# Kernel tuning notes

Measured on AMD Instinct MI355X. Metric: run time of the kernel, lower is better.

Reference implementation:

```python
import jax, jax.numpy as jnp
import numpy as np

B, N = 32, 512
NB_TAU, NB_G, NB_W = 8, 8, 6
FLOOR = 0.001
SLOPE_RANGE = (0.5, 4.0)
BIAS_RANGE = (-2.0, 2.0)


def _basis(x, nb, kind):
    # MonotoneBasis: fixed grid of slopes/biases, monotone activation per basis.
    slopes = jnp.asarray(np.linspace(SLOPE_RANGE[0], SLOPE_RANGE[1], nb), x.dtype)
    biases = jnp.asarray(np.linspace(BIAS_RANGE[0], BIAS_RANGE[1], nb), x.dtype)
    z = x[..., None] * slopes + biases  # [..., nb]
    return jax.nn.softplus(z) if kind == 'softplus' else jax.nn.sigmoid(z)


def _normalize_scores(scores, mask, eps=1e-6):
    scores = jnp.where(mask, scores, 0.0)
    denom = jnp.clip(mask.sum(axis=1, keepdims=True), 1)
    mean = scores.sum(axis=1, keepdims=True) / denom
    scores = scores - mean
    var = (scores ** 2 * mask).sum(axis=1, keepdims=True) / denom
    return scores / jnp.sqrt(var + eps)


def setup_inputs() -> dict:
    key = jax.random.key(0)
    k1, k2, k3, k4, k5 = jax.random.split(key, 5)
    return {
        'predictions': jax.random.normal(k1, (B, N), dtype=jnp.float32),
        # targets in [0,1): all valid (no -1 padding), ties have measure zero
        'targets': jax.random.uniform(k2, (B, N), dtype=jnp.float32),
        'theta_tau': jax.random.normal(k3, (NB_TAU,), dtype=jnp.float32) * 0.1,
        'theta_g': jax.random.normal(k4, (NB_G,), dtype=jnp.float32) * 0.1,
        'theta_w': jax.random.normal(k5, (NB_W,), dtype=jnp.float32) * 0.1,
    }


def reference(predictions, targets, theta_tau, theta_g, theta_w):
    mask = ~jnp.isclose(targets, -1.0)
    s = _normalize_scores(predictions, mask)
    r = targets
    n = predictions.shape[1]
    iu, ju = np.triu_indices(n, k=1)  # static pair enumeration, P = n*(n-1)/2

    dr = r[:, iu] - r[:, ju]                      # [B, P]
    t = jnp.sign(dr)
    keep = (t != 0) & mask[:, iu] & mask[:, ju]   # drop ties / padded pairs
    ds = s[:, iu] - s[:, ju]
    abs_dr = jnp.abs(dr)

    # learned nonnegative combination coefficients (monotone outputs)
    c_tau = jax.nn.softplus(theta_tau)
    c_g = jax.nn.softplus(theta_g)
    c_w = jax.nn.softplus(theta_w)

    tau = _basis(abs_dr, NB_TAU, 'softplus') @ c_tau   # learned margin
    m = tau - t * ds
    g = _basis(m, NB_G, 'softplus') @ c_g              # learned penalty
    w = FLOOR + _basis(abs_dr, NB_W, 'sigmoid') @ c_w  # learned gap weight
    pair_loss = g * w

    kf = keep.astype(pair_loss.dtype)
    denom = jnp.clip(kf.sum(axis=1), 1.0)
    row_loss = (pair_loss * kf).sum(axis=1) / denom    # per-row mean over kept pairs
    valid_row = (kf.sum(axis=1) > 0).astype(pair_loss.dtype)
    return (row_loss * valid_row).sum() / jnp.clip(valid_row.sum(), 1.0)
```

## Files before the change

### kernel.cpp

```cpp
#include <hip/hip_runtime.h>
#include <math.h>

#define BB 32
#define NN 512
#define PP 130816
#define KBLK 64
#define TAILSUB (KBLK - 2)

#define OFF_RS2 0
#define OFF_CF  32768
#define OFF_SUM 32816
#define OFF_CNT 32848

__device__ __forceinline__ float splus(float z) {
    return fmaxf(z, 0.0f) + __logf(1.0f + __expf(-fabsf(z)));
}

__device__ __constant__ float ST8[8] = {0.5f, 1.0f, 1.5f, 2.0f, 2.5f, 3.0f, 3.5f, 4.0f};
__device__ __constant__ float BT8[8] = {
    (float)(-2.0), (float)(-2.0 + 4.0/7.0), (float)(-2.0 + 8.0/7.0),
    (float)(-2.0 + 12.0/7.0), (float)(-2.0 + 16.0/7.0),
    (float)(-2.0 + 20.0/7.0), (float)(-2.0 + 24.0/7.0), 2.0f };
__device__ __constant__ float SW6[6] = {0.5f, (float)(0.5 + 3.5/5.0), (float)(0.5 + 7.0/5.0),
    (float)(0.5 + 10.5/5.0), (float)(0.5 + 14.0/5.0), 4.0f};
__device__ __constant__ float BW6[6] = {-2.0f, (float)(-2.0 + 4.0/5.0), (float)(-2.0 + 8.0/5.0),
    (float)(-2.0 + 12.0/5.0), (float)(-2.0 + 16.0/5.0), 2.0f};

__device__ __constant__ float TC[10][10] = {
    {1,0,0,0,0,0,0,0,0,0},
    {0,1,0,0,0,0,0,0,0,0},
    {-1,0,2,0,0,0,0,0,0,0},
    {0,-3,0,4,0,0,0,0,0,0},
    {1,0,-8,0,8,0,0,0,0,0},
    {0,5,0,-20,0,16,0,0,0,0},
    {-1,0,18,0,-48,0,32,0,0,0},
    {0,-7,0,56,0,-112,0,64,0,0},
    {1,0,-32,0,160,0,-256,0,128,0},
    {0,9,0,-120,0,432,0,-576,0,256},
};

__global__ __launch_bounds__(256)
void prep_kernel(const float* __restrict__ pred, const float* __restrict__ targ,
                 const float* __restrict__ th_tau, const float* __restrict__ th_g,
                 const float* __restrict__ th_w, float* __restrict__ ws)
{
    const int bid = blockIdx.x, tid = threadIdx.x;
    if (bid < BB) {
        const int base = bid * NN;
        float x0 = pred[base + tid], x1 = pred[base + tid + 256];
        float t0 = targ[base + tid], t1 = targ[base + tid + 256];
        bool v0 = fabsf(t0 + 1.0f) > 1.00001e-5f;
        bool v1 = fabsf(t1 + 1.0f) > 1.00001e-5f;
        float m0 = v0 ? 1.0f : 0.0f, m1 = v1 ? 1.0f : 0.0f;
        float xs0 = x0 * m0, xs1 = x1 * m1;
        float lsum = xs0 + xs1;
        float lsq  = xs0 * xs0 + xs1 * xs1;
        float lcnt = m0 + m1;
        #pragma unroll
        for (int off = 32; off; off >>= 1) {
            lsum += __shfl_down(lsum, off);
            lsq  += __shfl_down(lsq,  off);
            lcnt += __shfl_down(lcnt, off);
        }
        __shared__ float red[3][4];
        const int lane = tid & 63, wv = tid >> 6;
        if (lane == 0) { red[0][wv] = lsum; red[1][wv] = lsq; red[2][wv] = lcnt; }
        __syncthreads();
        __shared__ float mean_s, rsig_s;
        if (tid == 0) {
            float S = 0.0f, Q = 0.0f, C = 0.0f;
            for (int i = 0; i < 4; i++) { S += red[0][i]; Q += red[1][i]; C += red[2][i]; }
            float denom = fmaxf(C, 1.0f);
            float mean = S / denom;
            float var = Q / denom - mean * mean;
            mean_s = mean;
            rsig_s = 1.0f / sqrtf(var + 1e-6f);
            ws[OFF_SUM + bid] = 0.0f;
            ws[OFF_CNT + bid] = 0.0f;
        }
        __syncthreads();
        const float qnan = __uint_as_float(0x7fc00000u);
        float2* RS2 = (float2*)(ws + OFF_RS2);
        RS2[base + tid]       = make_float2(v0 ? t0 : qnan, (xs0 - mean_s) * rsig_s);
        RS2[base + tid + 256] = make_float2(v1 ? t1 : qnan, (xs1 - mean_s) * rsig_s);
    } else {
        const int wv = tid >> 6, lane = tid & 63;
        __shared__ float fbuf[4][64];
        __shared__ float cbuf[4][10];
        const float mids[4]  = {0.5f, 0.5f, -8.0f, 8.0f};
        const float halfs[4] = {0.5f, 0.5f,  8.0f, 8.0f};
        const int   ncs[4]   = {6, 6, 10, 10};
        const int   bases[4] = {0, 6, 12, 22};
        float u = __cosf((float)M_PI * ((float)lane + 0.5f) * (1.0f / 64.0f));
        float xv = fmaf(halfs[wv], u, mids[wv]);
        float f;
        if (wv == 0) {
            f = 0.0f;
            #pragma unroll
            for (int k = 0; k < 8; k++)
                f = fmaf(splus(fmaf(xv, ST8[k], BT8[k])), splus(th_tau[k]), f);
        } else if (wv == 1) {
            f = 0.001f;
            #pragma unroll
            for (int k = 0; k < 6; k++) {
                float z = fmaf(xv, SW6[k], BW6[k]);
                f = fmaf(1.0f / (1.0f + __expf(-z)), splus(th_w[k]), f);
            }
        } else {
            f = 0.0f;
            #pragma unroll
            for (int k = 0; k < 8; k++)
                f = fmaf(splus(fmaf(xv, ST8[k], BT8[k])), splus(th_g[k]), f);
        }
        fbuf[wv][lane] = f;
        __syncthreads();
        const int nc = ncs[wv];
        if (lane < nc) {
            float c = 0.0f;
            for (int i = 0; i < 64; i++)
                c += fbuf[wv][i] * __cosf((float)M_PI * (float)lane * ((float)i + 0.5f) * (1.0f / 64.0f));
            c *= (lane == 0) ? (1.0f / 64.0f) : (2.0f / 64.0f);
            cbuf[wv][lane] = c;
        }
        __syncthreads();
        if (lane < nc) {
            float mono = 0.0f;
            for (int j = 0; j < nc; j++) mono += cbuf[wv][j] * TC[j][lane];
            ws[OFF_CF + bases[wv] + lane] = mono;
        }
        if (wv == 2 && lane == 0) {
            float gB = 0.0f;
            #pragma unroll
            for (int k = 0; k < 8; k++) gB += splus(th_g[k]) * ST8[k];
            ws[OFF_CF + 32] = gB;
        }
    }
}

__global__ __launch_bounds__(256)
void pair_kernel(float* __restrict__ ws)
{
    const int b   = blockIdx.x & (BB - 1);
    const int sub = blockIdx.x >> 5;
    const int tid = threadIdx.x;
    __shared__ float2 sRS[NN];

    const float2* RS2 = (const float2*)(ws + OFF_RS2);
    sRS[tid]       = RS2[b * NN + tid];
    sRS[tid + 256] = RS2[b * NN + tid + 256];

    float ct[6], cw[6], cn[10], cp[10];
    #pragma unroll
    for (int k = 0; k < 6; k++)  ct[k] = ws[OFF_CF + k];
    #pragma unroll
    for (int k = 0; k < 6; k++)  cw[k] = ws[OFF_CF + 6 + k];
    #pragma unroll
    for (int k = 0; k < 10; k++) cn[k] = ws[OFF_CF + 12 + k];
    #pragma unroll
    for (int k = 0; k < 10; k++) cp[k] = ws[OFF_CF + 22 + k];
    const float gB = ws[OFF_CF + 32];
    __syncthreads();

    float lsum = 0.0f, lcnt = 0.0f;

    auto do_pair = [&](float2 a, float2 q) {
        float dr  = a.x - q.x;
        float ds  = a.y - q.y;
        float tds = __uint_as_float(__float_as_uint(ds) ^
                                    (__float_as_uint(dr) & 0x80000000u));
        float t1  = fmaf(fabsf(dr), 2.0f, -1.0f);
        float tau = fmaf(ct[5], t1, ct[4]);
        tau = fmaf(tau, t1, ct[3]); tau = fmaf(tau, t1, ct[2]);
        tau = fmaf(tau, t1, ct[1]); tau = fmaf(tau, t1, ct[0]);
        float w = fmaf(cw[5], t1, cw[4]);
        w = fmaf(w, t1, cw[3]); w = fmaf(w, t1, cw[2]);
        w = fmaf(w, t1, cw[1]); w = fmaf(w, t1, cw[0]);
        float m  = tau - tds;
        float um = fminf(fmaxf(m, -16.0f), 16.0f);
        bool neg = m < 0.0f;
        float tg = fmaf(um, 0.125f, neg ? 1.0f : -1.0f);
        float g = neg ? cn[9] : cp[9];
        #pragma unroll
        for (int k = 8; k >= 0; k--)
            g = fmaf(g, tg, neg ? cn[k] : cp[k]);
        g = fmaf(fmaxf(m - 16.0f, 0.0f), gB, g);
        float p = g * w;
        bool keep = __builtin_islessgreater(dr, 0.0f);
        lsum = keep ? (lsum + p) : lsum;
        lcnt = keep ? (lcnt + 1.0f) : lcnt;
    };

    const int d0 = (sub >> 1) + 1;
    const int x  = ((sub & 1) << 8) + tid;
    const float2 rsi = sRS[x];
    int j = (x + d0) & (NN - 1);
    const int nIter = (sub >= TAILSUB) ? (PP / (KBLK * 256) - 1) : (PP / (KBLK * 256));
    for (int it = 0; it < nIter; it++) {
        float2 rsj = sRS[j];
        do_pair(rsi, rsj);
        j = (j + 32) & (NN - 1);
    }
    if (sub == TAILSUB) {
        do_pair(sRS[tid], sRS[tid + 256]);
    }

    #pragma unroll
    for (int off = 32; off; off >>= 1) {
        lsum += __shfl_down(lsum, off);
        lcnt += __shfl_down(lcnt, off);
    }
    __shared__ float red[2][4];
    const int lane = tid & 63, wv = tid >> 6;
    if (lane == 0) { red[0][wv] = lsum; red[1][wv] = lcnt; }
    __syncthreads();
    if (tid == 0) {
        float S = red[0][0] + red[0][1] + red[0][2] + red[0][3];
        float C = red[1][0] + red[1][1] + red[1][2] + red[1][3];
        atomicAdd(ws + OFF_SUM + b, S);
        atomicAdd(ws + OFF_CNT + b, C);
    }
}

__global__ void final_kernel(const float* __restrict__ ws, float* __restrict__ out)
{
    const int tid = threadIdx.x;
    float val = 0.0f, vld = 0.0f;
    if (tid < BB) {
        float c = ws[OFF_CNT + tid], s = ws[OFF_SUM + tid];
        float rl = s / fmaxf(c, 1.0f);
        float v  = (c > 0.0f) ? 1.0f : 0.0f;
        val = rl * v;
        vld = v;
    }
    #pragma unroll
    for (int off = 32; off; off >>= 1) {
        val += __shfl_down(val, off);
        vld += __shfl_down(vld, off);
    }
    if (tid == 0) out[0] = val / fmaxf(vld, 1.0f);
}

extern "C" void kernel_launch(void* const* d_in, const int* in_sizes, int n_in,
                              void* d_out, int out_size, void* d_ws, size_t ws_size,
                              hipStream_t stream) {
    const float* pred   = (const float*)d_in[0];
    const float* targ   = (const float*)d_in[1];
    const float* th_tau = (const float*)d_in[2];
    const float* th_g   = (const float*)d_in[3];
    const float* th_w   = (const float*)d_in[4];
    float* ws  = (float*)d_ws;
    float* out = (float*)d_out;

    prep_kernel<<<BB + 1, 256, 0, stream>>>(pred, targ, th_tau, th_g, th_w, ws);
    pair_kernel<<<BB * KBLK, 256, 0, stream>>>(ws);
    final_kernel<<<1, 64, 0, stream>>>(ws, out);
}
```

Measured before the change: 86.62 us.

## Split g polynomial into even/odd parts and reshape pair enumeration

Replaces the sign-dependent Chebyshev selection for g with even and odd polynomial fits in |m|, so two independent Horner chains are combined by a sign flip. This removes the per-coefficient selects, which diverge inside a wavefront. Pair enumeration now uses a 768-entry wrapped shared array and 32 blocks per row, each with 16 fully unrolled contiguous offsets, in place of the modular stride loop and separate tail block. Fewer blocks and more work per thread cut launch and reduction overhead, but the doubled Horner FMA count adds ALU work.

Result: faster. 76.74 us (-11.4%).

```diff
diff --git a/kernel.cpp b/kernel.cpp
--- a/kernel.cpp
+++ b/kernel.cpp
@@ -3,14 +3,11 @@
 
 #define BB 32
 #define NN 512
-#define PP 130816
-#define KBLK 64
-#define TAILSUB (KBLK - 2)
 
 #define OFF_RS2 0
 #define OFF_CF  32768
-#define OFF_SUM 32816
-#define OFF_CNT 32848
+#define OFF_SUM 32808
+#define OFF_CNT 32840
 
 __device__ __forceinline__ float splus(float z) {
     return fmaxf(z, 0.0f) + __logf(1.0f + __expf(-fabsf(z)));
@@ -87,19 +84,16 @@
         const int wv = tid >> 6, lane = tid & 63;
         __shared__ float fbuf[4][64];
         __shared__ float cbuf[4][10];
-        const float mids[4]  = {0.5f, 0.5f, -8.0f, 8.0f};
-        const float halfs[4] = {0.5f, 0.5f,  8.0f, 8.0f};
-        const int   ncs[4]   = {6, 6, 10, 10};
-        const int   bases[4] = {0, 6, 12, 22};
         float u = __cosf((float)M_PI * ((float)lane + 0.5f) * (1.0f / 64.0f));
-        float xv = fmaf(halfs[wv], u, mids[wv]);
         float f;
         if (wv == 0) {
+            float xv = fmaf(0.5f, u, 0.5f);
             f = 0.0f;
             #pragma unroll
             for (int k = 0; k < 8; k++)
                 f = fmaf(splus(fmaf(xv, ST8[k], BT8[k])), splus(th_tau[k]), f);
         } else if (wv == 1) {
+            float xv = fmaf(0.5f, u, 0.5f);
             f = 0.001f;
             #pragma unroll
             for (int k = 0; k < 6; k++) {
@@ -107,14 +101,20 @@
                 f = fmaf(1.0f / (1.0f + __expf(-z)), splus(th_w[k]), f);
             }
         } else {
-            f = 0.0f;
-            #pragma unroll
-            for (int k = 0; k < 8; k++)
-                f = fmaf(splus(fmaf(xv, ST8[k], BT8[k])), splus(th_g[k]), f);
+            float xv = fmaf(8.0f, u, 8.0f);
+            float gp = 0.0f, gn = 0.0f;
+            #pragma unroll
+            for (int k = 0; k < 8; k++) {
+                float c = splus(th_g[k]);
+                gp = fmaf(splus(fmaf( xv, ST8[k], BT8[k])), c, gp);
+                gn = fmaf(splus(fmaf(-xv, ST8[k], BT8[k])), c, gn);
+            }
+            f = (wv == 2) ? 0.5f * (gp + gn) : 0.5f * (gp - gn);
         }
         fbuf[wv][lane] = f;
         __syncthreads();
-        const int nc = ncs[wv];
+        const int nc   = (wv < 2) ? 6 : 10;
+        const int base = (wv == 0) ? 0 : (wv == 1) ? 6 : (wv == 2) ? 12 : 22;
         if (lane < nc) {
             float c = 0.0f;
             for (int i = 0; i < 64; i++)
@@ -126,7 +126,7 @@
         if (lane < nc) {
             float mono = 0.0f;
             for (int j = 0; j < nc; j++) mono += cbuf[wv][j] * TC[j][lane];
-            ws[OFF_CF + bases[wv] + lane] = mono;
+            ws[OFF_CF + base + lane] = mono;
         }
         if (wv == 2 && lane == 0) {
             float gB = 0.0f;
@@ -138,36 +138,36 @@
 }
 
 __global__ __launch_bounds__(256)
-void pair_kernel(float* __restrict__ ws)
+void pair_kernel(const float2* __restrict__ RS2, const float* __restrict__ CF,
+                 float* __restrict__ sums)
 {
     const int b   = blockIdx.x & (BB - 1);
     const int sub = blockIdx.x >> 5;
     const int tid = threadIdx.x;
-    __shared__ float2 sRS[NN];
-
-    const float2* RS2 = (const float2*)(ws + OFF_RS2);
+    __shared__ float2 sRS[768];
     sRS[tid]       = RS2[b * NN + tid];
     sRS[tid + 256] = RS2[b * NN + tid + 256];
-
-    float ct[6], cw[6], cn[10], cp[10];
-    #pragma unroll
-    for (int k = 0; k < 6; k++)  ct[k] = ws[OFF_CF + k];
-    #pragma unroll
-    for (int k = 0; k < 6; k++)  cw[k] = ws[OFF_CF + 6 + k];
-    #pragma unroll
-    for (int k = 0; k < 10; k++) cn[k] = ws[OFF_CF + 12 + k];
-    #pragma unroll
-    for (int k = 0; k < 10; k++) cp[k] = ws[OFF_CF + 22 + k];
-    const float gB = ws[OFF_CF + 32];
+    sRS[tid + 512] = RS2[b * NN + tid];
+
+    float ct[6], cw[6], ce[10], co[10];
+    #pragma unroll
+    for (int k = 0; k < 6; k++)  ct[k] = CF[k];
+    #pragma unroll
+    for (int k = 0; k < 6; k++)  cw[k] = CF[6 + k];
+    #pragma unroll
+    for (int k = 0; k < 10; k++) ce[k] = CF[12 + k];
+    #pragma unroll
+    for (int k = 0; k < 10; k++) co[k] = CF[22 + k];
+    const float gB = CF[32];
     __syncthreads();
 
     float lsum = 0.0f, lcnt = 0.0f;
 
-    auto do_pair = [&](float2 a, float2 q) {
+    auto do_pair = [&](float2 a, float2 q, bool allow) {
         float dr  = a.x - q.x;
         float ds  = a.y - q.y;
-        float tds = __uint_as_float(__float_as_uint(ds) ^
-                                    (__float_as_uint(dr) & 0x80000000u));
+        unsigned sgn = __float_as_uint(dr) & 0x80000000u;
+        float tds = __uint_as_float(__float_as_uint(ds) ^ sgn);
         float t1  = fmaf(fabsf(dr), 2.0f, -1.0f);
         float tau = fmaf(ct[5], t1, ct[4]);
         tau = fmaf(tau, t1, ct[3]); tau = fmaf(tau, t1, ct[2]);
@@ -176,33 +176,36 @@
         w = fmaf(w, t1, cw[3]); w = fmaf(w, t1, cw[2]);
         w = fmaf(w, t1, cw[1]); w = fmaf(w, t1, cw[0]);
         float m  = tau - tds;
-        float um = fminf(fmaxf(m, -16.0f), 16.0f);
-        bool neg = m < 0.0f;
-        float tg = fmaf(um, 0.125f, neg ? 1.0f : -1.0f);
-        float g = neg ? cn[9] : cp[9];
+        float au = fminf(fabsf(m), 16.0f);
+        float tg = fmaf(au, 0.125f, -1.0f);
+        float E = ce[9], O = co[9];
         #pragma unroll
-        for (int k = 8; k >= 0; k--)
-            g = fmaf(g, tg, neg ? cn[k] : cp[k]);
+        for (int k = 8; k >= 0; k--) {
+            E = fmaf(E, tg, ce[k]);
+            O = fmaf(O, tg, co[k]);
+        }
+        unsigned msgn = __float_as_uint(m) & 0x80000000u;
+        float g = E + __uint_as_float(__float_as_uint(O) ^ msgn);
         g = fmaf(fmaxf(m - 16.0f, 0.0f), gB, g);
         float p = g * w;
-        bool keep = __builtin_islessgreater(dr, 0.0f);
+        bool keep = __builtin_islessgreater(dr, 0.0f) && allow;
         lsum = keep ? (lsum + p) : lsum;
         lcnt = keep ? (lcnt + 1.0f) : lcnt;
     };
 
-    const int d0 = (sub >> 1) + 1;
-    const int x  = ((sub & 1) << 8) + tid;
-    const float2 rsi = sRS[x];
-    int j = (x + d0) & (NN - 1);
-    const int nIter = (sub >= TAILSUB) ? (PP / (KBLK * 256) - 1) : (PP / (KBLK * 256));
-    for (int it = 0; it < nIter; it++) {
-        float2 rsj = sRS[j];
-        do_pair(rsi, rsj);
-        j = (j + 32) & (NN - 1);
-    }
-    if (sub == TAILSUB) {
-        do_pair(sRS[tid], sRS[tid + 256]);
-    }
+    const int d0 = sub * 8 + 1;
+    const float2 a0 = sRS[tid];
+    const float2 a1 = sRS[tid + 256];
+    const float2* pj0 = &sRS[tid + d0];
+    const float2* pj1 = &sRS[tid + 256 + d0];
+    const bool lastsub = (sub == 31);
+    #pragma unroll
+    for (int k = 0; k < 8; k++)
+        do_pair(a0, pj0[k], true);
+    #pragma unroll
+    for (int k = 0; k < 7; k++)
+        do_pair(a1, pj1[k], true);
+    do_pair(a1, pj1[7], !lastsub);
 
     #pragma unroll
     for (int off = 32; off; off >>= 1) {
@@ -216,17 +219,17 @@
     if (tid == 0) {
         float S = red[0][0] + red[0][1] + red[0][2] + red[0][3];
         float C = red[1][0] + red[1][1] + red[1][2] + red[1][3];
-        atomicAdd(ws + OFF_SUM + b, S);
-        atomicAdd(ws + OFF_CNT + b, C);
-    }
-}
-
-__global__ void final_kernel(const float* __restrict__ ws, float* __restrict__ out)
+        atomicAdd(sums + b, S);
+        atomicAdd(sums + BB + b, C);
+    }
+}
+
+__global__ void final_kernel(const float* __restrict__ sums, float* __restrict__ out)
 {
     const int tid = threadIdx.x;
     float val = 0.0f, vld = 0.0f;
     if (tid < BB) {
-        float c = ws[OFF_CNT + tid], s = ws[OFF_SUM + tid];
+        float s = sums[tid], c = sums[BB + tid];
         float rl = s / fmaxf(c, 1.0f);
         float v  = (c > 0.0f) ? 1.0f : 0.0f;
         val = rl * v;
@@ -252,6 +255,7 @@
     float* out = (float*)d_out;
 
     prep_kernel<<<BB + 1, 256, 0, stream>>>(pred, targ, th_tau, th_g, th_w, ws);
-    pair_kernel<<<BB * KBLK, 256, 0, stream>>>(ws);
-    final_kernel<<<1, 64, 0, stream>>>(ws, out);
-}
+    pair_kernel<<<BB * 32, 256, 0, stream>>>((const float2*)(ws + OFF_RS2),
+                                             ws + OFF_CF, ws + OFF_SUM);
+    final_kernel<<<1, 64, 0, stream>>>(ws + OFF_SUM, out);
+}
```
